# Kernel optimization log

Hardware: AMD Instinct MI355X
Metric: run time of the kernel (lower is better)

The kernel has to match this reference:

```python
import jax, jax.numpy as jnp
import numpy as np

B, G, K, N = 8, 2048, 32, 6
C = 64  # lc_x feature dim (mapping_size), must be even
SCALE = 10.0
EPS = 1e-8


def setup_inputs() -> dict:
    key = jax.random.key(0)
    k1, k2, k3 = jax.random.split(key, 3)
    lc_x = jax.random.normal(k1, (B, G, C), dtype=jnp.float32)
    knn_x = jax.random.normal(k2, (B, G, K, N), dtype=jnp.float32)
    fourier_B = jax.random.normal(k3, (7, C // 2), dtype=jnp.float32) * SCALE
    return {"lc_x": lc_x, "knn_x": knn_x, "fourier_B": fourier_B}


def reference(lc_x, knn_x, fourier_B):
    # lc_x: [B,G,C], knn_x: [B,G,K,N], fourier_B: [7, C//2]
    lc_normal = lc_x[:, :, 3:6][:, :, None, :]            # [B,G,1,3], broadcasts over K
    lc_line = lc_x / jnp.linalg.norm(lc_x, axis=2, keepdims=True)
    lc_line = jnp.transpose(lc_line, (0, 2, 1))            # [B,C,G]

    knn_product = knn_x[..., 3:6]                          # [B,G,K,3]
    lcn_b = jnp.broadcast_to(lc_normal, knn_product.shape)
    knn_cross = jnp.cross(knn_product, lcn_b, axis=-1)     # [B,G,K,3]
    knn_dot = jnp.sum(knn_product * lc_normal, axis=-1, keepdims=True)  # [B,G,K,1]
    knn_line = jnp.concatenate([knn_product, knn_cross, knn_dot], axis=-1)  # [B,G,K,7]

    # Fourier feature mapping (4D path: permute to channels-last already holds)
    x_proj = knn_line @ fourier_B                          # [B,G,K,C/2]
    ff = jnp.concatenate([jnp.sin(2 * jnp.pi * x_proj), jnp.cos(2 * jnp.pi * x_proj)], axis=-1)
    ff = jnp.sign(ff) * jnp.abs(ff) ** 5                   # [B,G,K,C]
    knn_f = jnp.transpose(ff, (0, 3, 1, 2))                # [B,C,G,K]

    # K_ANP over last dim (K); torch.std is unbiased (ddof=1); .item() -> stop_gradient
    std = jnp.std(knn_f, axis=-1, keepdims=True, ddof=1)
    p = 2.0 + jax.lax.stop_gradient(jnp.log1p(jnp.mean(std)))
    norm = jnp.sum(jnp.abs(knn_f) ** p, axis=-1, keepdims=True) ** (1.0 / p)  # [B,C,G,1]
    lc = norm / (norm + EPS)  # sum over size-1 last dim equals norm itself
    e_x = jnp.exp(lc)                                      # [B,C,G,1]
    up = jnp.mean(knn_f * e_x, axis=-1)                    # [B,C,G]
    down = jnp.mean(e_x, axis=-1)                          # [B,C,G]
    anp = up / down

    kl = anp + jnp.mean(knn_f, axis=-1)                    # [B,C,G] (squeeze is no-op: B,C,G>1)
    kl = kl / jnp.linalg.norm(kl, axis=-1, keepdims=True)  # normalize over G
    line_element = kl - lc_line
    return jnp.concatenate([line_element, lc_line], axis=1)  # [B,2C,G]
```

## Files before the change

kernel.cpp:

```cpp
#include <hip/hip_runtime.h>
#include <hip/hip_bf16.h>


#if __has_builtin(__builtin_amdgcn_fractf)
  #define FRACT(x) __builtin_amdgcn_fractf(x)
#else
  #define FRACT(x) ((x) - floorf(x))
#endif

__device__ __forceinline__ float rlanef(float v, int l) {
    return __int_as_float(__builtin_amdgcn_readlane(__float_as_int(v), l));
}

__device__ __forceinline__ float wave_sum64(float v) {
    float s = v;
    s += __int_as_float(__builtin_amdgcn_update_dpp(
            0, __float_as_int(s), 0x111, 0xf, 0xf, true));
    s += __int_as_float(__builtin_amdgcn_update_dpp(
            0, __float_as_int(s), 0x112, 0xf, 0xf, true));
    s += __int_as_float(__builtin_amdgcn_update_dpp(
            0, __float_as_int(s), 0x114, 0xf, 0xf, true));
    s += __int_as_float(__builtin_amdgcn_update_dpp(
            0, __float_as_int(s), 0x118, 0xf, 0xf, true));
    s += __int_as_float(__builtin_amdgcn_update_dpp(
            0, __float_as_int(s), 0x142, 0xf, 0xf, true));
    s += __int_as_float(__builtin_amdgcn_update_dpp(
            0, __float_as_int(s), 0x143, 0xf, 0xf, true));
    return rlanef(s, 63);
}

__global__ __launch_bounds__(256, 8) void line_pass1(
    const float* __restrict__ lc_x,
    const float* __restrict__ knn_x,
    const float* __restrict__ fB,
    float* __restrict__ out)
{
    const int wave = threadIdx.x >> 6;
    const int lane = threadIdx.x & 63;
    const int half = lane >> 5;
    const int jj   = lane & 31;
    const int sbid = (blockIdx.x & 7) * 256 + (blockIdx.x >> 3);
    const int bg0  = sbid * 8;
    const int b    = bg0 >> 11;
    const int g0   = bg0 & 2047;

    __shared__ __align__(16) float4 pbuf[4][2][32];
    __shared__ float klbuf[128][9];

    const float fb0 = fB[0*32 + jj];
    const float fb1 = fB[1*32 + jj];
    const float fb2 = fB[2*32 + jj];
    const float fb3 = fB[3*32 + jj];
    const float fb4 = fB[4*32 + jj];
    const float fb5 = fB[5*32 + jj];
    const float fb6 = fB[6*32 + jj];

    const int bgw = bg0 + wave * 2;
    const float myv0 = lc_x[(size_t)bgw * 64 + lane];
    const float myv1 = lc_x[(size_t)(bgw + 1) * 64 + lane];
    {
        const float* kp = knn_x + (size_t)(bgw + half) * 192 + jj * 6;
        pbuf[wave][half][jj] = make_float4(kp[3], kp[4], kp[5], 0.0f);
    }
    asm volatile("s_waitcnt lgkmcnt(0)" ::: "memory");

    #pragma unroll
    for (int i = 0; i < 2; ++i) {
        const int col = wave * 2 + i;
        const float myv = (i == 0) ? myv0 : myv1;

        const float n0 = rlanef(myv, 3);
        const float n1 = rlanef(myv, 4);
        const float n2 = rlanef(myv, 5);

        const float ssum = wave_sum64(myv * myv);
        klbuf[64 + lane][col] = myv * __builtin_amdgcn_rsqf(ssum);

        const float e0 = fmaf(fb6, n0, fmaf(fb5,  n1, fmaf(fb4, -n2, fb0)));
        const float e1 = fmaf(fb6, n1, fmaf(fb5, -n0, fmaf(fb3,  n2, fb1)));
        const float e2 = fmaf(fb6, n2, fmaf(fb4,  n0, fmaf(fb3, -n1, fb2)));

        float accS0 = 0.f, accS1 = 0.f, accC0 = 0.f, accC1 = 0.f;
        const float4* myk = &pbuf[wave][i][half];
        #pragma unroll
        for (int t = 0; t < 16; ++t) {
            const float4 p = myk[2 * t];
            const float x  = fmaf(e2, p.z, fmaf(e1, p.y, e0 * p.x));
            const float ts = FRACT(x);
            const float s  = __builtin_amdgcn_sinf(ts);
            const float cq = __builtin_amdgcn_cosf(ts);
            const float s2 = s * s,   s4 = s2 * s2;
            const float q2 = cq * cq, q4 = q2 * q2;
            if (t & 1) { accS1 = fmaf(s4, s, accS1); accC1 = fmaf(q4, cq, accC1); }
            else       { accS0 = fmaf(s4, s, accS0); accC0 = fmaf(q4, cq, accC0); }
        }
        const float aS = accS0 + accS1;
        const float aC = accC0 + accC1;
        const float totS = aS + __shfl_xor(aS, 32, 64);
        const float totC = aC + __shfl_xor(aC, 32, 64);
        klbuf[lane][col] = (half ? totC : totS) * 0.0625f;
    }

    __syncthreads();

    const int c  = threadIdx.x >> 1;
    const int j0 = (threadIdx.x & 1) * 4;
    const float4 o = make_float4(klbuf[c][j0], klbuf[c][j0+1],
                                 klbuf[c][j0+2], klbuf[c][j0+3]);
    *(float4*)(out + ((size_t)b * 128 + c) * 2048 + g0 + j0) = o;
}

__global__ __launch_bounds__(256) void line_pass2(float* __restrict__ out)
{
    const int b = blockIdx.x >> 6;
    const int c = blockIdx.x & 63;
    float4*       kl = (float4*)(out + ((size_t)b * 128 + c) * 2048);
    const float4* ll = (const float4*)(out + ((size_t)b * 128 + 64 + c) * 2048);
    const int t = threadIdx.x;

    const float4 v0 = kl[t];
    const float4 v1 = kl[t + 256];
    const float4 l0 = ll[t];
    const float4 l1 = ll[t + 256];

    float ss = v0.x*v0.x + v0.y*v0.y + v0.z*v0.z + v0.w*v0.w
             + v1.x*v1.x + v1.y*v1.y + v1.z*v1.z + v1.w*v1.w;
    #pragma unroll
    for (int off = 32; off; off >>= 1) ss += __shfl_xor(ss, off, 64);

    __shared__ float wsum[4];
    if ((t & 63) == 0) wsum[t >> 6] = ss;
    __syncthreads();
    const float tot = wsum[0] + wsum[1] + wsum[2] + wsum[3];
    const float rn  = __builtin_amdgcn_rsqf(tot);

    kl[t]       = make_float4(fmaf(v0.x, rn, -l0.x), fmaf(v0.y, rn, -l0.y),
                              fmaf(v0.z, rn, -l0.z), fmaf(v0.w, rn, -l0.w));
    kl[t + 256] = make_float4(fmaf(v1.x, rn, -l1.x), fmaf(v1.y, rn, -l1.y),
                              fmaf(v1.z, rn, -l1.z), fmaf(v1.w, rn, -l1.w));
}

extern "C" void kernel_launch(void* const* d_in, const int* in_sizes, int n_in,
                              void* d_out, int out_size, void* d_ws, size_t ws_size,
                              hipStream_t stream) {
    const float* lc_x  = (const float*)d_in[0];
    const float* knn_x = (const float*)d_in[1];
    const float* fB    = (const float*)d_in[2];
    float* out = (float*)d_out;

    line_pass1<<<2048, 256, 0, stream>>>(lc_x, knn_x, fB, out);
    line_pass2<<<512, 256, 0, stream>>>(out);
}
```

Before: 19.51 us.

## Accumulate per-channel sum of squares with atomics in pass1, simplify pass2

```diff
diff --git a/kernel.cpp b/kernel.cpp
--- a/kernel.cpp
+++ b/kernel.cpp
@@ -33,7 +33,8 @@
     const float* __restrict__ lc_x,
     const float* __restrict__ knn_x,
     const float* __restrict__ fB,
-    float* __restrict__ out)
+    float* __restrict__ out,
+    float* __restrict__ ws)
 {
     const int wave = threadIdx.x >> 6;
     const int lane = threadIdx.x & 63;
@@ -64,6 +65,7 @@
     }
     asm volatile("s_waitcnt lgkmcnt(0)" ::: "memory");
 
+    float kv[2];
     #pragma unroll
     for (int i = 0; i < 2; ++i) {
         const int col = wave * 2 + i;
@@ -98,8 +100,11 @@
         const float aC = accC0 + accC1;
         const float totS = aS + __shfl_xor(aS, 32, 64);
         const float totC = aC + __shfl_xor(aC, 32, 64);
-        klbuf[lane][col] = (half ? totC : totS) * 0.0625f;
+        kv[i] = (half ? totC : totS);
+        klbuf[lane][col] = kv[i];
     }
+
+    atomicAdd(&ws[b * 64 + lane], fmaf(kv[0], kv[0], kv[1] * kv[1]));
 
     __syncthreads();
 
@@ -110,34 +115,23 @@
     *(float4*)(out + ((size_t)b * 128 + c) * 2048 + g0 + j0) = o;
 }
 
-__global__ __launch_bounds__(256) void line_pass2(float* __restrict__ out)
+__global__ __launch_bounds__(256) void line_pass2(
+    float* __restrict__ out, const float* __restrict__ ws)
 {
-    const int b = blockIdx.x >> 6;
-    const int c = blockIdx.x & 63;
-    float4*       kl = (float4*)(out + ((size_t)b * 128 + c) * 2048);
-    const float4* ll = (const float4*)(out + ((size_t)b * 128 + 64 + c) * 2048);
-    const int t = threadIdx.x;
+    const int i   = blockIdx.x * 256 + threadIdx.x;
+    const int row = i >> 9;
+    const int b   = row >> 6;
+    const int c   = row & 63;
+    const int q   = i & 511;
 
-    const float4 v0 = kl[t];
-    const float4 v1 = kl[t + 256];
-    const float4 l0 = ll[t];
-    const float4 l1 = ll[t + 256];
+    float4*       kl = (float4*)(out + ((size_t)b * 128 + c) * 2048) + q;
+    const float4* ll = (const float4*)(out + ((size_t)b * 128 + 64 + c) * 2048) + q;
 
-    float ss = v0.x*v0.x + v0.y*v0.y + v0.z*v0.z + v0.w*v0.w
-             + v1.x*v1.x + v1.y*v1.y + v1.z*v1.z + v1.w*v1.w;
-    #pragma unroll
-    for (int off = 32; off; off >>= 1) ss += __shfl_xor(ss, off, 64);
-
-    __shared__ float wsum[4];
-    if ((t & 63) == 0) wsum[t >> 6] = ss;
-    __syncthreads();
-    const float tot = wsum[0] + wsum[1] + wsum[2] + wsum[3];
-    const float rn  = __builtin_amdgcn_rsqf(tot);
-
-    kl[t]       = make_float4(fmaf(v0.x, rn, -l0.x), fmaf(v0.y, rn, -l0.y),
-                              fmaf(v0.z, rn, -l0.z), fmaf(v0.w, rn, -l0.w));
-    kl[t + 256] = make_float4(fmaf(v1.x, rn, -l1.x), fmaf(v1.y, rn, -l1.y),
-                              fmaf(v1.z, rn, -l1.z), fmaf(v1.w, rn, -l1.w));
+    const float rn = __builtin_amdgcn_rsqf(ws[row]);
+    const float4 v = *kl;
+    const float4 l = *ll;
+    *kl = make_float4(fmaf(v.x, rn, -l.x), fmaf(v.y, rn, -l.y),
+                      fmaf(v.z, rn, -l.z), fmaf(v.w, rn, -l.w));
 }
 
 extern "C" void kernel_launch(void* const* d_in, const int* in_sizes, int n_in,
@@ -147,7 +141,9 @@
     const float* knn_x = (const float*)d_in[1];
     const float* fB    = (const float*)d_in[2];
     float* out = (float*)d_out;
+    float* ws  = (float*)d_ws;
 
-    line_pass1<<<2048, 256, 0, stream>>>(lc_x, knn_x, fB, out);
-    line_pass2<<<512, 256, 0, stream>>>(out);
+    hipMemsetAsync(d_ws, 0, 512 * sizeof(float), stream);
+    line_pass1<<<2048, 256, 0, stream>>>(lc_x, knn_x, fB, out, ws);
+    line_pass2<<<1024, 256, 0, stream>>>(out, ws);
 }
```

Result: slower. 44.72 us (+129.2%).
